# Kernel tuning notes

Measured on AMD Instinct MI355X. Metric: run time of the kernel, lower is better.

## Reference

```python
import jax, jax.numpy as jnp
import numpy as np
import math

H = 128  # hidden_dim
RADIUS = 30.0


def _lin(x, w, b):
    return x @ w + b


def _masked_softmax(logits, mask):
    return jax.nn.softmax(jnp.where(mask, logits, -1e9), axis=-1)


def setup_inputs() -> dict:
    key = jax.random.key(0)
    ks = iter(jax.random.split(key, 64))

    def p(shape, s=0.02):
        return (jax.random.normal(next(ks), shape, jnp.float32) * s)

    B, N, T, M, L = 2, 48, 24, 192, 20
    inp = {
        'agents_state': jax.random.normal(next(ks), (B, N, T, 5), jnp.float32),
        'agents_mask': jnp.ones((B, N, T), jnp.float32),
        'map_polylines': jax.random.normal(next(ks), (B, M, L, 2), jnp.float32),
        'map_poly_mask': jnp.ones((B, M), jnp.float32),
        'map_poly_type': jax.random.randint(next(ks), (B, M), 0, 4),
        'map_tl_status': jax.random.randint(next(ks), (B, M), 0, 8),
        'map_on_route': jax.random.randint(next(ks), (B, M), 0, 2),
        # AgentStateEncoder
        'ae_w0': p((5, H)), 'ae_b0': p((H,)), 'ae_w1': p((H, H)), 'ae_b1': p((H,)),
        'ae_w2': p((H, H)), 'ae_b2': p((H,)),
        # MapPolylineNodeEncoder point_mlp
        'mp_w0': p((2, H)), 'mp_b0': p((H,)), 'mp_w1': p((H, H)), 'mp_b1': p((H,)),
        'type_emb': p((4, H)), 'tl_emb': p((8, H)), 'route_emb': p((2, H)),
        'mo_w0': p((H, H)), 'mo_b0': p((H,)), 'mo_w1': p((H, H)), 'mo_b1': p((H,)),
        # map_rel_mlp (3 -> H -> 1)
        'mr_w0': p((3, H)), 'mr_b0': p((H,)), 'mr_w1': p((H, 1)), 'mr_b1': p((1,)),
        # nbr_rel_mlp (5 -> H -> 1)
        'nr_w0': p((5, H)), 'nr_b0': p((H,)), 'nr_w1': p((H, 1)), 'nr_b1': p((1,)),
        # tau_out (3H -> H -> 64)
        'to_w0': p((3 * H, H)), 'to_b0': p((H,)), 'to_w1': p((H, 64)), 'to_b1': p((64,)),
    }
    return inp


def reference(agents_state, agents_mask, map_polylines, map_poly_mask,
              map_poly_type, map_tl_status, map_on_route,
              ae_w0, ae_b0, ae_w1, ae_b1, ae_w2, ae_b2,
              mp_w0, mp_b0, mp_w1, mp_b1, type_emb, tl_emb, route_emb,
              mo_w0, mo_b0, mo_w1, mo_b1,
              mr_w0, mr_b0, mr_w1, mr_b1,
              nr_w0, nr_b0, nr_w1, nr_b1,
              to_w0, to_b0, to_w1, to_b1):
    B, N, T, _ = agents_state.shape
    a_mask = agents_mask > 0.5
    a_feat = agents_state[..., :5]

    # --- MapPolylineNodeEncoder ---
    m = map_poly_mask > 0.5
    h = jax.nn.relu(_lin(jax.nn.relu(_lin(map_polylines, mp_w0, mp_b0)), mp_w1, mp_b1))  # B,M,L,H
    h = h.max(axis=2)  # B,M,H
    pt = jnp.clip(map_poly_type, 0, type_emb.shape[0] - 1)
    tl = jnp.clip(map_tl_status, 0, tl_emb.shape[0] - 1)
    rt = jnp.clip(map_on_route, 0, route_emb.shape[0] - 1)
    h = h + type_emb[pt] + tl_emb[tl] + route_emb[rt]
    h = _lin(jax.nn.relu(_lin(h, mo_w0, mo_b0)), mo_w1, mo_b1)
    map_node = h * m[..., None].astype(h.dtype)  # B,M,D
    map_center = map_polylines.mean(axis=2)  # B,M,2

    # --- AgentStateEncoder ---
    a = jax.nn.relu(_lin(a_feat, ae_w0, ae_b0))
    a = jax.nn.relu(_lin(a, ae_w1, ae_b1))
    a_emb = _lin(a, ae_w2, ae_b2) * a_mask[..., None].astype(a.dtype)  # B,N,T,D

    # --- map cross-attention with relative-position bias ---
    agent_pos = a_feat[..., 0:2]
    rel = map_center[:, None, None, :, :] - agent_pos[:, :, :, None, :]  # B,N,T,M,2
    dist = jnp.linalg.norm(rel, axis=-1, keepdims=True)
    rel_feat = jnp.concatenate([rel, dist], axis=-1)  # B,N,T,M,3
    rel_score = _lin(jax.nn.relu(_lin(rel_feat, mr_w0, mr_b0)), mr_w1, mr_b1)[..., 0]  # B,N,T,M
    dot = jnp.einsum('bntd,bmd->bntm', a_emb, map_node) / math.sqrt(map_node.shape[-1])
    attn = _masked_softmax(dot + rel_score, m[:, None, None, :])
    map_ctx = jnp.einsum('bntm,bmd->bntd', attn, map_node)

    # --- neighbor graph attention ---
    pos = a_feat[..., 0:2]
    vel = a_feat[..., 3:5]
    rel_pos = jnp.transpose(pos[:, :, None] - pos[:, None, :], (0, 1, 3, 2, 4))  # B,N,T,N,2
    rel_vel = jnp.transpose(vel[:, :, None] - vel[:, None, :], (0, 1, 3, 2, 4))
    dist_ij = jnp.linalg.norm(rel_pos, axis=-1, keepdims=True)  # B,N,T,N,1
    rel_ij = jnp.concatenate([rel_pos, rel_vel, dist_ij], axis=-1)  # B,N,T,N,5
    nbr_score = _lin(jax.nn.relu(_lin(rel_ij, nr_w0, nr_b0)), nr_w1, nr_b1)[..., 0]  # B,N,T,N

    valid_i = a_mask[..., None]  # B,N,T,1
    valid_j = jnp.transpose(a_mask, (0, 2, 1))[:, None, :, :]  # B,1,T,N
    radius_ok = dist_ij[..., 0] <= RADIUS
    not_self = ~jnp.eye(N, dtype=bool)[None, :, None, :]  # 1,N,1,N
    nbr_mask = valid_i & valid_j & radius_ok & not_self

    dot_n = jnp.einsum('bntd,bjtd->bntj', a_emb, a_emb) / math.sqrt(a_emb.shape[-1])
    w_n = _masked_softmax(dot_n + nbr_score, nbr_mask)  # B,N,T,N
    nbr_ctx = jnp.einsum('bntj,bjtd->bntd', w_n, a_emb)

    tau = jnp.concatenate([a_emb, map_ctx, nbr_ctx], axis=-1)
    tau = _lin(jax.nn.relu(_lin(tau, to_w0, to_b0)), to_w1, to_b1)
    tau = tau * a_mask[..., None].astype(tau.dtype)
    return tau, map_ctx, nbr_ctx
```

## Files before the change

### kernel.cpp

```cpp
#include <hip/hip_runtime.h>
#include <math.h>

#define HH 128
#define BB 2
#define NN 48
#define TT 24
#define MM 192
#define LL 20
#define NT (BB*NN*TT)
#define RSQRT_H 0.08838834764831845f
#define RADIUS_C 30.0f

struct P {
    const float *astate, *amask, *polylines, *poly_mask;
    const int *ptype, *tlst, *route;
    const float *ae_w0,*ae_b0,*ae_w1,*ae_b1,*ae_w2,*ae_b2;
    const float *mp_w0,*mp_b0,*mp_w1,*mp_b1;
    const float *type_emb,*tl_emb,*route_emb;
    const float *mo_w0,*mo_b0,*mo_w1,*mo_b1;
    const float *mr_w0,*mr_b0,*mr_w1,*mr_b1;
    const float *nr_w0,*nr_b0,*nr_w1,*nr_b1;
    const float *to_w0,*to_b0,*to_w1,*to_b1;
    float *tau,*map_ctx,*nbr_ctx;
    float *a_emb,*map_node,*map_nodeT,*map_center;
};

struct SME { float pts[LL*2]; float h1[LL][HH]; float mx[2][HH]; float hb[HH]; float pr[2][HH]; float hb2[HH]; };
struct SAG { float xin[4][5]; float h1[4][HH]; float h2[4][HH]; float p1[2][4][HH]; };

struct SF {
    float4 aq4L[HH];
    float  mctx[4][HH];
    float  nctx[4][HH];
    float  pc[2][4][HH];
    union {
        struct {
            float  mnL[16][MM];
            float4 w4L[HH];
            float  w1L[HH];
            float  lg[4][MM];
            float4 p4L[MM];
            float  invL[4];
        } m;
        struct {
            float  pjL[NN][8];
            float4 wAL[HH];
            float4 wBL[HH];
            float  sPL[4][4][NN];
            float  dPL[4][4][NN];
            float  lgN[4][NN];
            float4 pN[NN];
        } n;
        struct {
            float  xinT[3*HH][4];
            float  h1T[HH][4];
        } t;
    } u;
};

__device__ void do_map_enc(const P& p, SME& s, int bm) {
    int tid = threadIdx.x, pp = tid >> 7, c = tid & 127;
    if (tid < LL*2) s.pts[tid] = p.polylines[(size_t)bm*LL*2 + tid];
    __syncthreads();
    {
        float w0x = p.mp_w0[c], w0y = p.mp_w0[HH + c], b0 = p.mp_b0[c];
        #pragma unroll
        for (int i = 0; i < 10; ++i) {
            int pt_ = pp + 2*i;
            s.h1[pt_][c] = fmaxf(fmaf(s.pts[2*pt_], w0x, fmaf(s.pts[2*pt_+1], w0y, b0)), 0.f);
        }
    }
    if (tid < 2) {
        float sum = 0.f;
        for (int q = 0; q < LL; ++q) sum += s.pts[2*q + tid];
        p.map_center[bm*2 + tid] = sum * (1.0f / LL);
    }
    __syncthreads();
    {
        float acc[10];
        float b1 = p.mp_b1[c];
        #pragma unroll
        for (int i = 0; i < 10; ++i) acc[i] = b1;
        for (int k = 0; k < HH; ++k) {
            float wv = p.mp_w1[k*HH + c];
            #pragma unroll
            for (int i = 0; i < 10; ++i) acc[i] = fmaf(s.h1[pp + 2*i][k], wv, acc[i]);
        }
        float m10 = acc[0];
        #pragma unroll
        for (int i = 1; i < 10; ++i) m10 = fmaxf(m10, acc[i]);
        s.mx[pp][c] = m10;
    }
    __syncthreads();
    if (tid < HH) {
        float hm = fmaxf(fmaxf(s.mx[0][c], s.mx[1][c]), 0.f);
        int pt = p.ptype[bm]; pt = pt < 0 ? 0 : (pt > 3 ? 3 : pt);
        int tv = p.tlst[bm];  tv = tv < 0 ? 0 : (tv > 7 ? 7 : tv);
        int rv = p.route[bm]; rv = rv < 0 ? 0 : (rv > 1 ? 1 : rv);
        hm += p.type_emb[pt*HH + c] + p.tl_emb[tv*HH + c] + p.route_emb[rv*HH + c];
        s.hb[c] = hm;
    }
    __syncthreads();
    {
        float sum = 0.f;
        int k0 = pp*64;
        for (int k = k0; k < k0 + 64; ++k) sum = fmaf(s.hb[k], p.mo_w0[k*HH + c], sum);
        s.pr[pp][c] = sum;
    }
    __syncthreads();
    if (tid < HH) s.hb2[c] = fmaxf(s.pr[0][c] + s.pr[1][c] + p.mo_b0[c], 0.f);
    __syncthreads();
    {
        float sum = 0.f;
        int k0 = pp*64;
        for (int k = k0; k < k0 + 64; ++k) sum = fmaf(s.hb2[k], p.mo_w1[k*HH + c], sum);
        s.pr[pp][c] = sum;
    }
    __syncthreads();
    if (tid < HH) {
        float a3 = s.pr[0][c] + s.pr[1][c] + p.mo_b1[c];
        float mk = (p.poly_mask[bm] > 0.5f) ? 1.f : 0.f;
        float v = a3 * mk;
        p.map_node[(size_t)bm*HH + c] = v;
        int b = bm / MM, m = bm % MM;
        p.map_nodeT[((size_t)b*HH + c)*MM + m] = v;
    }
}

__device__ void do_agent_enc(const P& p, SAG& s, int r0) {
    int tid = threadIdx.x, h = tid >> 7, c = tid & 127;
    if (tid < 20) s.xin[tid/5][tid%5] = p.astate[(size_t)r0*5 + tid];
    __syncthreads();
    if (h == 0) {
        float b = p.ae_b0[c];
        float w[5];
        #pragma unroll
        for (int i = 0; i < 5; ++i) w[i] = p.ae_w0[i*HH + c];
        #pragma unroll
        for (int r = 0; r < 4; ++r) {
            float v = b;
            #pragma unroll
            for (int i = 0; i < 5; ++i) v = fmaf(s.xin[r][i], w[i], v);
            s.h1[r][c] = fmaxf(v, 0.f);
        }
    }
    __syncthreads();
    {
        float acc[4] = {0.f,0.f,0.f,0.f};
        int k0 = h*64;
        for (int k = k0; k < k0 + 64; ++k) {
            float wv = p.ae_w1[k*HH + c];
            #pragma unroll
            for (int r = 0; r < 4; ++r) acc[r] = fmaf(s.h1[r][k], wv, acc[r]);
        }
        #pragma unroll
        for (int r = 0; r < 4; ++r) s.p1[h][r][c] = acc[r];
    }
    __syncthreads();
    {
        #pragma unroll
        for (int rr = 0; rr < 2; ++rr) {
            int r = h*2 + rr;
            s.h2[r][c] = fmaxf(s.p1[0][r][c] + s.p1[1][r][c] + p.ae_b1[c], 0.f);
        }
    }
    __syncthreads();
    {
        float acc[4] = {0.f,0.f,0.f,0.f};
        int k0 = h*64;
        for (int k = k0; k < k0 + 64; ++k) {
            float wv = p.ae_w2[k*HH + c];
            #pragma unroll
            for (int r = 0; r < 4; ++r) acc[r] = fmaf(s.h2[r][k], wv, acc[r]);
        }
        #pragma unroll
        for (int r = 0; r < 4; ++r) s.p1[h][r][c] = acc[r];
    }
    __syncthreads();
    {
        #pragma unroll
        for (int rr = 0; rr < 2; ++rr) {
            int r = h*2 + rr;
            int row = r0 + r;
            p.a_emb[(size_t)row*HH + c] = (s.p1[0][r][c] + s.p1[1][r][c] + p.ae_b2[c]) * p.amask[row];
        }
    }
}

__global__ __launch_bounds__(256) void k_enc(P p) {
    __shared__ __align__(16) char smraw[(sizeof(SME) > sizeof(SAG)) ? sizeof(SME) : sizeof(SAG)];
    int task = blockIdx.x;
    if (task < BB*MM) do_map_enc(p, *(SME*)smraw, task);
    else              do_agent_enc(p, *(SAG*)smraw, (task - BB*MM)*4);
}

__global__ __launch_bounds__(256) void k_fat(P p) {
    __shared__ __align__(16) SF s;
    int task = blockIdx.x;
    int b    = task / (TT*12);
    int rem  = task % (TT*12);
    int t    = rem / 12;
    int n0   = (rem % 12) * 4;
    int tid  = threadIdx.x;

    int row0 = (b*NN + n0)*TT + t;

    for (int idx = tid; idx < 4*HH; idx += 256) {
        int r = idx >> 7, k = idx & 127;
        ((float*)&s.aq4L[k])[r] = p.a_emb[(size_t)(row0 + r*TT)*HH + k];
    }
    if (tid < HH) {
        int k = tid;
        s.u.m.w4L[k] = make_float4(p.mr_w0[k], p.mr_w0[HH+k], p.mr_w0[2*HH+k], p.mr_b0[k]);
        s.u.m.w1L[k] = p.mr_w1[k];
    }

    float rx[4], ry[4], rd[4];
    if (tid < MM) {
        float mcx = p.map_center[(b*MM + tid)*2];
        float mcy = p.map_center[(b*MM + tid)*2 + 1];
        #pragma unroll
        for (int r = 0; r < 4; ++r) {
            float px = p.astate[(size_t)(row0 + r*TT)*5];
            float py = p.astate[(size_t)(row0 + r*TT)*5 + 1];
            rx[r] = mcx - px; ry[r] = mcy - py;
            rd[r] = sqrtf(rx[r]*rx[r] + ry[r]*ry[r]);
        }
    }

    const float* mnT = p.map_nodeT + (size_t)b*HH*MM;
    float4 st[3];
    #pragma unroll
    for (int i = 0; i < 3; ++i) {
        int q = tid + 256*i;
        int kk = q / 48, mq = q % 48;
        st[i] = *(const float4*)(mnT + (size_t)kk*MM + mq*4);
    }
    float sacc[4] = {0.f,0.f,0.f,0.f};
    float dt4[4]  = {0.f,0.f,0.f,0.f};
    for (int ch = 0; ch < 8; ++ch) {
        __syncthreads();
        #pragma unroll
        for (int i = 0; i < 3; ++i) {
            int q = tid + 256*i;
            int kk = q / 48, mq = q % 48;
            *(float4*)&s.u.m.mnL[kk][mq*4] = st[i];
        }
        __syncthreads();
        if (ch < 7) {
            #pragma unroll
            for (int i = 0; i < 3; ++i) {
                int q = tid + 256*i;
                int kk = q / 48, mq = q % 48;
                st[i] = *(const float4*)(mnT + (size_t)(ch+1)*16*MM + (size_t)kk*MM + mq*4);
            }
        }
        if (tid < MM) {
            int k0 = ch*16;
            #pragma unroll
            for (int kk = 0; kk < 16; ++kk) {
                int k = k0 + kk;
                float4 w  = s.u.m.w4L[k];
                float  w1 = s.u.m.w1L[k];
                float4 aq = s.aq4L[k];
                float  mn = s.u.m.mnL[kk][tid];
                #pragma unroll
                for (int r = 0; r < 4; ++r) {
                    float hv = fmaf(rx[r], w.x, fmaf(ry[r], w.y, fmaf(rd[r], w.z, w.w)));
                    sacc[r] = fmaf(fmaxf(hv, 0.f), w1, sacc[r]);
                }
                dt4[0] = fmaf(aq.x, mn, dt4[0]);
                dt4[1] = fmaf(aq.y, mn, dt4[1]);
                dt4[2] = fmaf(aq.z, mn, dt4[2]);
                dt4[3] = fmaf(aq.w, mn, dt4[3]);
            }
        }
    }
    if (tid < MM) {
        float pm = p.poly_mask[b*MM + tid];
        float b1 = p.mr_b1[0];
        #pragma unroll
        for (int r = 0; r < 4; ++r) {
            float lgt = fmaf(dt4[r], RSQRT_H, sacc[r] + b1);
            s.u.m.lg[r][tid] = (pm > 0.5f) ? lgt : -1e9f;
        }
    }
    __syncthreads();

    {
        int r = tid >> 6, l = tid & 63;
        float v = fmaxf(fmaxf(s.u.m.lg[r][l], s.u.m.lg[r][l+64]), s.u.m.lg[r][l+128]);
        #pragma unroll
        for (int o = 32; o > 0; o >>= 1) v = fmaxf(v, __shfl_xor(v, o));
        float e0 = expf(s.u.m.lg[r][l] - v);
        float e1 = expf(s.u.m.lg[r][l+64] - v);
        float e2 = expf(s.u.m.lg[r][l+128] - v);
        s.u.m.lg[r][l] = e0; s.u.m.lg[r][l+64] = e1; s.u.m.lg[r][l+128] = e2;
        float sm = e0 + e1 + e2;
        #pragma unroll
        for (int o = 32; o > 0; o >>= 1) sm += __shfl_xor(sm, o);
        if (l == 0) s.u.m.invL[r] = 1.0f / sm;
    }
    __syncthreads();
    if (tid < MM) {
        s.u.m.p4L[tid] = make_float4(s.u.m.lg[0][tid]*s.u.m.invL[0], s.u.m.lg[1][tid]*s.u.m.invL[1],
                                     s.u.m.lg[2][tid]*s.u.m.invL[2], s.u.m.lg[3][tid]*s.u.m.invL[3]);
    }
    __syncthreads();

    {
        int half = tid >> 7, c = tid & 127;
        float a0=0.f, a1=0.f, a2=0.f, a3=0.f;
        const float* mnb = p.map_node + ((size_t)b*MM + half*96)*HH + c;
        for (int m = 0; m < 96; ++m) {
            float mv = mnb[(size_t)m*HH];
            float4 pp4 = s.u.m.p4L[half*96 + m];
            a0 = fmaf(pp4.x, mv, a0); a1 = fmaf(pp4.y, mv, a1);
            a2 = fmaf(pp4.z, mv, a2); a3 = fmaf(pp4.w, mv, a3);
        }
        s.pc[half][0][c]=a0; s.pc[half][1][c]=a1; s.pc[half][2][c]=a2; s.pc[half][3][c]=a3;
    }
    __syncthreads();
    for (int idx = tid; idx < 4*HH; idx += 256) {
        int r = idx >> 7, c = idx & 127;
        float v = s.pc[0][r][c] + s.pc[1][r][c];
        s.mctx[r][c] = v;
        p.map_ctx[(size_t)(row0 + r*TT)*HH + c] = v;
    }
    __syncthreads();

    if (tid < NN) {
        int rj = (b*NN + tid)*TT + t;
        s.u.n.pjL[tid][0] = p.astate[(size_t)rj*5];
        s.u.n.pjL[tid][1] = p.astate[(size_t)rj*5 + 1];
        s.u.n.pjL[tid][2] = p.astate[(size_t)rj*5 + 3];
        s.u.n.pjL[tid][3] = p.astate[(size_t)rj*5 + 4];
        s.u.n.pjL[tid][4] = p.amask[rj];
    }
    if (tid < HH) {
        int k = tid;
        s.u.n.wAL[k] = make_float4(p.nr_w0[k], p.nr_w0[HH+k], p.nr_w0[2*HH+k], p.nr_w0[3*HH+k]);
        s.u.n.wBL[k] = make_float4(p.nr_w0[4*HH+k], p.nr_b0[k], p.nr_w1[k], 0.f);
    }
    __syncthreads();

    {
        int j  = tid % 48;
        int kg = tid / 48;
        if (kg < 4) {
            float jx = s.u.n.pjL[j][0], jy = s.u.n.pjL[j][1];
            float jvx = s.u.n.pjL[j][2], jvy = s.u.n.pjL[j][3];
            float dx[4], dy[4], dvx[4], dvy[4], dd[4];
            #pragma unroll
            for (int r = 0; r < 4; ++r) {
                int ni = n0 + r;
                dx[r]  = s.u.n.pjL[ni][0] - jx;  dy[r]  = s.u.n.pjL[ni][1] - jy;
                dvx[r] = s.u.n.pjL[ni][2] - jvx; dvy[r] = s.u.n.pjL[ni][3] - jvy;
                dd[r]  = sqrtf(dx[r]*dx[r] + dy[r]*dy[r]);
            }
            const float* aj = p.a_emb + ((size_t)(b*NN + j)*TT + t)*HH;
            float sr[4]  = {0,0,0,0};
            float dtn[4] = {0,0,0,0};
            int k0 = kg*32;
            for (int kk = 0; kk < 32; ++kk) {
                int k = k0 + kk;
                float4 wa = s.u.n.wAL[k], wb = s.u.n.wBL[k];
                float4 aq = s.aq4L[k];
                float  av = aj[k];
                #pragma unroll
                for (int r = 0; r < 4; ++r) {
                    float hv = fmaf(dx[r], wa.x, fmaf(dy[r], wa.y,
                               fmaf(dvx[r], wa.z, fmaf(dvy[r], wa.w,
                               fmaf(dd[r], wb.x, wb.y)))));
                    sr[r] = fmaf(fmaxf(hv, 0.f), wb.z, sr[r]);
                }
                dtn[0] = fmaf(aq.x, av, dtn[0]); dtn[1] = fmaf(aq.y, av, dtn[1]);
                dtn[2] = fmaf(aq.z, av, dtn[2]); dtn[3] = fmaf(aq.w, av, dtn[3]);
            }
            #pragma unroll
            for (int r = 0; r < 4; ++r) { s.u.n.sPL[kg][r][j] = sr[r]; s.u.n.dPL[kg][r][j] = dtn[r]; }
        }
    }
    __syncthreads();

    {
        float b1 = p.nr_b1[0];
        for (int idx = tid; idx < 4*NN; idx += 256) {
            int r = idx / NN, jj = idx % NN;
            int ni = n0 + r;
            float ss  = s.u.n.sPL[0][r][jj] + s.u.n.sPL[1][r][jj] + s.u.n.sPL[2][r][jj] + s.u.n.sPL[3][r][jj] + b1;
            float do2 = s.u.n.dPL[0][r][jj] + s.u.n.dPL[1][r][jj] + s.u.n.dPL[2][r][jj] + s.u.n.dPL[3][r][jj];
            float ddx = s.u.n.pjL[ni][0] - s.u.n.pjL[jj][0];
            float ddy = s.u.n.pjL[ni][1] - s.u.n.pjL[jj][1];
            float dist = sqrtf(ddx*ddx + ddy*ddy);
            bool ok = (s.u.n.pjL[ni][4] > 0.5f) && (s.u.n.pjL[jj][4] > 0.5f) &&
                      (dist <= RADIUS_C) && (jj != ni);
            s.u.n.lgN[r][jj] = ok ? fmaf(do2, RSQRT_H, ss) : -1e9f;
        }
    }
    __syncthreads();

    {
        int r = tid >> 6, l = tid & 63;
        float v = (l < NN) ? s.u.n.lgN[r][l] : -3.4e38f;
        #pragma unroll
        for (int o = 32; o > 0; o >>= 1) v = fmaxf(v, __shfl_xor(v, o));
        float e = (l < NN) ? expf(s.u.n.lgN[r][l] - v) : 0.f;
        float sm = e;
        #pragma unroll
        for (int o = 32; o > 0; o >>= 1) sm += __shfl_xor(sm, o);
        if (l < NN) s.u.n.lgN[r][l] = e / sm;
    }
    __syncthreads();
    if (tid < NN) {
        s.u.n.pN[tid] = make_float4(s.u.n.lgN[0][tid], s.u.n.lgN[1][tid],
                                    s.u.n.lgN[2][tid], s.u.n.lgN[3][tid]);
    }
    __syncthreads();

    {
        int half = tid >> 7, c = tid & 127;
        float a0=0.f, a1=0.f, a2=0.f, a3=0.f;
        for (int jj = half*24; jj < half*24 + 24; ++jj) {
            float av = p.a_emb[((size_t)(b*NN + jj)*TT + t)*HH + c];
            float4 pp4 = s.u.n.pN[jj];
            a0 = fmaf(pp4.x, av, a0); a1 = fmaf(pp4.y, av, a1);
            a2 = fmaf(pp4.z, av, a2); a3 = fmaf(pp4.w, av, a3);
        }
        s.pc[half][0][c]=a0; s.pc[half][1][c]=a1; s.pc[half][2][c]=a2; s.pc[half][3][c]=a3;
    }
    __syncthreads();
    for (int idx = tid; idx < 4*HH; idx += 256) {
        int r = idx >> 7, c = idx & 127;
        float v = s.pc[0][r][c] + s.pc[1][r][c];
        s.nctx[r][c] = v;
        p.nbr_ctx[(size_t)(row0 + r*TT)*HH + c] = v;
    }
    __syncthreads();

    for (int idx = tid; idx < 4*HH; idx += 256) {
        int r = idx >> 7, k = idx & 127;
        s.u.t.xinT[k][r]        = ((float*)&s.aq4L[k])[r];
        s.u.t.xinT[HH + k][r]   = s.mctx[r][k];
        s.u.t.xinT[2*HH + k][r] = s.nctx[r][k];
    }
    __syncthreads();
    {
        int c = tid & 127, h = tid >> 7;
        float acc[4] = {0,0,0,0};
        for (int k = h*192; k < h*192 + 192; ++k) {
            float wv = p.to_w0[k*HH + c];
            float4 xa = *(const float4*)&s.u.t.xinT[k][0];
            acc[0]=fmaf(xa.x,wv,acc[0]); acc[1]=fmaf(xa.y,wv,acc[1]);
            acc[2]=fmaf(xa.z,wv,acc[2]); acc[3]=fmaf(xa.w,wv,acc[3]);
        }
        #pragma unroll
        for (int r = 0; r < 4; ++r) s.pc[h][r][c] = acc[r];
    }
    __syncthreads();
    for (int idx = tid; idx < 4*HH; idx += 256) {
        int r = idx >> 7, k = idx & 127;
        s.u.t.h1T[k][r] = fmaxf(s.pc[0][r][k] + s.pc[1][r][k] + p.to_b0[k], 0.f);
    }
    __syncthreads();
    {
        int r = tid >> 6, c2 = tid & 63;
        float acc = p.to_b1[c2];
        for (int k = 0; k < HH; ++k)
            acc = fmaf(s.u.t.h1T[k][r], p.to_w1[k*64 + c2], acc);
        p.tau[(size_t)(row0 + r*TT)*64 + c2] = acc * p.amask[row0 + r*TT];
    }
}

extern "C" void kernel_launch(void* const* d_in, const int* in_sizes, int n_in,
                              void* d_out, int out_size, void* d_ws, size_t ws_size,
                              hipStream_t stream)
{
    P p;
    p.astate    = (const float*)d_in[0];
    p.amask     = (const float*)d_in[1];
    p.polylines = (const float*)d_in[2];
    p.poly_mask = (const float*)d_in[3];
    p.ptype     = (const int*)d_in[4];
    p.tlst      = (const int*)d_in[5];
    p.route     = (const int*)d_in[6];
    p.ae_w0 = (const float*)d_in[7];  p.ae_b0 = (const float*)d_in[8];
    p.ae_w1 = (const float*)d_in[9];  p.ae_b1 = (const float*)d_in[10];
    p.ae_w2 = (const float*)d_in[11]; p.ae_b2 = (const float*)d_in[12];
    p.mp_w0 = (const float*)d_in[13]; p.mp_b0 = (const float*)d_in[14];
    p.mp_w1 = (const float*)d_in[15]; p.mp_b1 = (const float*)d_in[16];
    p.type_emb  = (const float*)d_in[17];
    p.tl_emb    = (const float*)d_in[18];
    p.route_emb = (const float*)d_in[19];
    p.mo_w0 = (const float*)d_in[20]; p.mo_b0 = (const float*)d_in[21];
    p.mo_w1 = (const float*)d_in[22]; p.mo_b1 = (const float*)d_in[23];
    p.mr_w0 = (const float*)d_in[24]; p.mr_b0 = (const float*)d_in[25];
    p.mr_w1 = (const float*)d_in[26]; p.mr_b1 = (const float*)d_in[27];
    p.nr_w0 = (const float*)d_in[28]; p.nr_b0 = (const float*)d_in[29];
    p.nr_w1 = (const float*)d_in[30]; p.nr_b1 = (const float*)d_in[31];
    p.to_w0 = (const float*)d_in[32]; p.to_b0 = (const float*)d_in[33];
    p.to_w1 = (const float*)d_in[34]; p.to_b1 = (const float*)d_in[35];

    p.tau     = (float*)d_out;
    p.map_ctx = (float*)d_out + (size_t)NT*64;
    p.nbr_ctx = p.map_ctx + (size_t)NT*HH;

    float* ws    = (float*)d_ws;
    p.a_emb      = ws;
    p.map_node   = p.a_emb + (size_t)NT*HH;
    p.map_nodeT  = p.map_node + (size_t)BB*MM*HH;
    p.map_center = p.map_nodeT + (size_t)BB*MM*HH;

    k_enc<<<BB*MM + NT/4, 256, 0, stream>>>(p);
    k_fat<<<BB*TT*12,     256, 0, stream>>>(p);
}
```

Baseline: 187.9 us.

## Halve rows per block to double grid size and drop shared map tiling

Each block in both kernels now handles 2 agent rows instead of 4, doubling the number of blocks (576 to 1152 for the fat kernel and more agent-encoder blocks) to fill more compute units. The map logit loop drops the staged shared-memory tiles of map_nodeT and reads it directly from global memory with coalesced per-thread loads. The final tau projection is split across both thread halves over k. This gives more parallelism and less shared memory per block, but weight loads are reused across fewer rows, so global and L2 traffic per output grows.

```diff
diff --git a/kernel.cpp b/kernel.cpp
--- a/kernel.cpp
+++ b/kernel.cpp
@@ -26,34 +26,33 @@
 };
 
 struct SME { float pts[LL*2]; float h1[LL][HH]; float mx[2][HH]; float hb[HH]; float pr[2][HH]; float hb2[HH]; };
-struct SAG { float xin[4][5]; float h1[4][HH]; float h2[4][HH]; float p1[2][4][HH]; };
+struct SAG { float xin[2][5]; float h1[2][HH]; float h2[2][HH]; float p1[2][2][HH]; };
 
 struct SF {
-    float4 aq4L[HH];
-    float  mctx[4][HH];
-    float  nctx[4][HH];
-    float  pc[2][4][HH];
+    float aqL[HH][2];
+    float mctx[2][HH];
+    float nctx[2][HH];
+    float pc[2][2][HH];
     union {
         struct {
-            float  mnL[16][MM];
             float4 w4L[HH];
             float  w1L[HH];
-            float  lg[4][MM];
-            float4 p4L[MM];
-            float  invL[4];
+            float  lg[2][MM];
+            float  p2[MM][2];
+            float  invL[2];
         } m;
         struct {
             float  pjL[NN][8];
             float4 wAL[HH];
             float4 wBL[HH];
-            float  sPL[4][4][NN];
-            float  dPL[4][4][NN];
-            float  lgN[4][NN];
-            float4 pN[NN];
+            float  sPL[4][2][NN];
+            float  dPL[4][2][NN];
+            float  lgN[2][NN];
+            float  pN[NN][2];
         } n;
         struct {
-            float  xinT[3*HH][4];
-            float  h1T[HH][4];
+            float  xinT[3*HH][2];
+            float  h1T[HH][2];
         } t;
     } u;
 };
@@ -129,7 +128,7 @@
 
 __device__ void do_agent_enc(const P& p, SAG& s, int r0) {
     int tid = threadIdx.x, h = tid >> 7, c = tid & 127;
-    if (tid < 20) s.xin[tid/5][tid%5] = p.astate[(size_t)r0*5 + tid];
+    if (tid < 10) s.xin[tid/5][tid%5] = p.astate[(size_t)r0*5 + tid];
     __syncthreads();
     if (h == 0) {
         float b = p.ae_b0[c];
@@ -137,7 +136,7 @@
         #pragma unroll
         for (int i = 0; i < 5; ++i) w[i] = p.ae_w0[i*HH + c];
         #pragma unroll
-        for (int r = 0; r < 4; ++r) {
+        for (int r = 0; r < 2; ++r) {
             float v = b;
             #pragma unroll
             for (int i = 0; i < 5; ++i) v = fmaf(s.xin[r][i], w[i], v);
@@ -146,44 +145,36 @@
     }
     __syncthreads();
     {
-        float acc[4] = {0.f,0.f,0.f,0.f};
+        float a0 = 0.f, a1 = 0.f;
         int k0 = h*64;
         for (int k = k0; k < k0 + 64; ++k) {
             float wv = p.ae_w1[k*HH + c];
-            #pragma unroll
-            for (int r = 0; r < 4; ++r) acc[r] = fmaf(s.h1[r][k], wv, acc[r]);
-        }
-        #pragma unroll
-        for (int r = 0; r < 4; ++r) s.p1[h][r][c] = acc[r];
-    }
-    __syncthreads();
-    {
-        #pragma unroll
-        for (int rr = 0; rr < 2; ++rr) {
-            int r = h*2 + rr;
-            s.h2[r][c] = fmaxf(s.p1[0][r][c] + s.p1[1][r][c] + p.ae_b1[c], 0.f);
-        }
-    }
-    __syncthreads();
-    {
-        float acc[4] = {0.f,0.f,0.f,0.f};
+            a0 = fmaf(s.h1[0][k], wv, a0);
+            a1 = fmaf(s.h1[1][k], wv, a1);
+        }
+        s.p1[h][0][c] = a0; s.p1[h][1][c] = a1;
+    }
+    __syncthreads();
+    {
+        int r = h;
+        s.h2[r][c] = fmaxf(s.p1[0][r][c] + s.p1[1][r][c] + p.ae_b1[c], 0.f);
+    }
+    __syncthreads();
+    {
+        float a0 = 0.f, a1 = 0.f;
         int k0 = h*64;
         for (int k = k0; k < k0 + 64; ++k) {
             float wv = p.ae_w2[k*HH + c];
-            #pragma unroll
-            for (int r = 0; r < 4; ++r) acc[r] = fmaf(s.h2[r][k], wv, acc[r]);
-        }
-        #pragma unroll
-        for (int r = 0; r < 4; ++r) s.p1[h][r][c] = acc[r];
-    }
-    __syncthreads();
-    {
-        #pragma unroll
-        for (int rr = 0; rr < 2; ++rr) {
-            int r = h*2 + rr;
-            int row = r0 + r;
-            p.a_emb[(size_t)row*HH + c] = (s.p1[0][r][c] + s.p1[1][r][c] + p.ae_b2[c]) * p.amask[row];
-        }
+            a0 = fmaf(s.h2[0][k], wv, a0);
+            a1 = fmaf(s.h2[1][k], wv, a1);
+        }
+        s.p1[h][0][c] = a0; s.p1[h][1][c] = a1;
+    }
+    __syncthreads();
+    {
+        int r = h;
+        int row = r0 + r;
+        p.a_emb[(size_t)row*HH + c] = (s.p1[0][r][c] + s.p1[1][r][c] + p.ae_b2[c]) * p.amask[row];
     }
 }
 
@@ -191,23 +182,23 @@
     __shared__ __align__(16) char smraw[(sizeof(SME) > sizeof(SAG)) ? sizeof(SME) : sizeof(SAG)];
     int task = blockIdx.x;
     if (task < BB*MM) do_map_enc(p, *(SME*)smraw, task);
-    else              do_agent_enc(p, *(SAG*)smraw, (task - BB*MM)*4);
+    else              do_agent_enc(p, *(SAG*)smraw, (task - BB*MM)*2);
 }
 
 __global__ __launch_bounds__(256) void k_fat(P p) {
     __shared__ __align__(16) SF s;
     int task = blockIdx.x;
-    int b    = task / (TT*12);
-    int rem  = task % (TT*12);
-    int t    = rem / 12;
-    int n0   = (rem % 12) * 4;
+    int b    = task / (TT*24);
+    int rem  = task % (TT*24);
+    int t    = rem / 24;
+    int n0   = (rem % 24) * 2;
     int tid  = threadIdx.x;
 
     int row0 = (b*NN + n0)*TT + t;
 
-    for (int idx = tid; idx < 4*HH; idx += 256) {
-        int r = idx >> 7, k = idx & 127;
-        ((float*)&s.aq4L[k])[r] = p.a_emb[(size_t)(row0 + r*TT)*HH + k];
+    for (int idx = tid; idx < 2*HH; idx += 256) {
+        int r = idx & 1, k = idx >> 1;
+        s.aqL[k][r] = p.a_emb[(size_t)(row0 + r*TT)*HH + k];
     }
     if (tid < HH) {
         int k = tid;
@@ -215,113 +206,86 @@
         s.u.m.w1L[k] = p.mr_w1[k];
     }
 
-    float rx[4], ry[4], rd[4];
+    float rx[2], ry[2], rd[2];
     if (tid < MM) {
         float mcx = p.map_center[(b*MM + tid)*2];
         float mcy = p.map_center[(b*MM + tid)*2 + 1];
         #pragma unroll
-        for (int r = 0; r < 4; ++r) {
+        for (int r = 0; r < 2; ++r) {
             float px = p.astate[(size_t)(row0 + r*TT)*5];
             float py = p.astate[(size_t)(row0 + r*TT)*5 + 1];
             rx[r] = mcx - px; ry[r] = mcy - py;
             rd[r] = sqrtf(rx[r]*rx[r] + ry[r]*ry[r]);
         }
     }
-
-    const float* mnT = p.map_nodeT + (size_t)b*HH*MM;
-    float4 st[3];
-    #pragma unroll
-    for (int i = 0; i < 3; ++i) {
-        int q = tid + 256*i;
-        int kk = q / 48, mq = q % 48;
-        st[i] = *(const float4*)(mnT + (size_t)kk*MM + mq*4);
-    }
-    float sacc[4] = {0.f,0.f,0.f,0.f};
-    float dt4[4]  = {0.f,0.f,0.f,0.f};
-    for (int ch = 0; ch < 8; ++ch) {
-        __syncthreads();
-        #pragma unroll
-        for (int i = 0; i < 3; ++i) {
-            int q = tid + 256*i;
-            int kk = q / 48, mq = q % 48;
-            *(float4*)&s.u.m.mnL[kk][mq*4] = st[i];
-        }
-        __syncthreads();
-        if (ch < 7) {
-            #pragma unroll
-            for (int i = 0; i < 3; ++i) {
-                int q = tid + 256*i;
-                int kk = q / 48, mq = q % 48;
-                st[i] = *(const float4*)(mnT + (size_t)(ch+1)*16*MM + (size_t)kk*MM + mq*4);
+    __syncthreads();
+
+    if (tid < MM) {
+        const float* mnc = p.map_nodeT + (size_t)b*HH*MM + tid;
+        float sacc[2] = {0.f, 0.f};
+        float dt2[2]  = {0.f, 0.f};
+        #pragma unroll 8
+        for (int k = 0; k < HH; ++k) {
+            float4 w  = s.u.m.w4L[k];
+            float  w1 = s.u.m.w1L[k];
+            float  mn = mnc[(size_t)k*MM];
+            float  aq0 = s.aqL[k][0], aq1 = s.aqL[k][1];
+            #pragma unroll
+            for (int r = 0; r < 2; ++r) {
+                float hv = fmaf(rx[r], w.x, fmaf(ry[r], w.y, fmaf(rd[r], w.z, w.w)));
+                sacc[r] = fmaf(fmaxf(hv, 0.f), w1, sacc[r]);
             }
-        }
-        if (tid < MM) {
-            int k0 = ch*16;
-            #pragma unroll
-            for (int kk = 0; kk < 16; ++kk) {
-                int k = k0 + kk;
-                float4 w  = s.u.m.w4L[k];
-                float  w1 = s.u.m.w1L[k];
-                float4 aq = s.aq4L[k];
-                float  mn = s.u.m.mnL[kk][tid];
-                #pragma unroll
-                for (int r = 0; r < 4; ++r) {
-                    float hv = fmaf(rx[r], w.x, fmaf(ry[r], w.y, fmaf(rd[r], w.z, w.w)));
-                    sacc[r] = fmaf(fmaxf(hv, 0.f), w1, sacc[r]);
-                }
-                dt4[0] = fmaf(aq.x, mn, dt4[0]);
-                dt4[1] = fmaf(aq.y, mn, dt4[1]);
-                dt4[2] = fmaf(aq.z, mn, dt4[2]);
-                dt4[3] = fmaf(aq.w, mn, dt4[3]);
-            }
-        }
-    }
-    if (tid < MM) {
+            dt2[0] = fmaf(aq0, mn, dt2[0]);
+            dt2[1] = fmaf(aq1, mn, dt2[1]);
+        }
         float pm = p.poly_mask[b*MM + tid];
         float b1 = p.mr_b1[0];
         #pragma unroll
-        for (int r = 0; r < 4; ++r) {
-            float lgt = fmaf(dt4[r], RSQRT_H, sacc[r] + b1);
+        for (int r = 0; r < 2; ++r) {
+            float lgt = fmaf(dt2[r], RSQRT_H, sacc[r] + b1);
             s.u.m.lg[r][tid] = (pm > 0.5f) ? lgt : -1e9f;
         }
     }
     __syncthreads();
 
     {
-        int r = tid >> 6, l = tid & 63;
-        float v = fmaxf(fmaxf(s.u.m.lg[r][l], s.u.m.lg[r][l+64]), s.u.m.lg[r][l+128]);
-        #pragma unroll
-        for (int o = 32; o > 0; o >>= 1) v = fmaxf(v, __shfl_xor(v, o));
-        float e0 = expf(s.u.m.lg[r][l] - v);
-        float e1 = expf(s.u.m.lg[r][l+64] - v);
-        float e2 = expf(s.u.m.lg[r][l+128] - v);
-        s.u.m.lg[r][l] = e0; s.u.m.lg[r][l+64] = e1; s.u.m.lg[r][l+128] = e2;
-        float sm = e0 + e1 + e2;
-        #pragma unroll
-        for (int o = 32; o > 0; o >>= 1) sm += __shfl_xor(sm, o);
-        if (l == 0) s.u.m.invL[r] = 1.0f / sm;
+        int w = tid >> 6, l = tid & 63;
+        if (w < 2) {
+            int r = w;
+            float v = fmaxf(fmaxf(s.u.m.lg[r][l], s.u.m.lg[r][l+64]), s.u.m.lg[r][l+128]);
+            #pragma unroll
+            for (int o = 32; o > 0; o >>= 1) v = fmaxf(v, __shfl_xor(v, o));
+            float e0 = expf(s.u.m.lg[r][l] - v);
+            float e1 = expf(s.u.m.lg[r][l+64] - v);
+            float e2 = expf(s.u.m.lg[r][l+128] - v);
+            s.u.m.lg[r][l] = e0; s.u.m.lg[r][l+64] = e1; s.u.m.lg[r][l+128] = e2;
+            float sm = e0 + e1 + e2;
+            #pragma unroll
+            for (int o = 32; o > 0; o >>= 1) sm += __shfl_xor(sm, o);
+            if (l == 0) s.u.m.invL[r] = 1.0f / sm;
+        }
     }
     __syncthreads();
     if (tid < MM) {
-        s.u.m.p4L[tid] = make_float4(s.u.m.lg[0][tid]*s.u.m.invL[0], s.u.m.lg[1][tid]*s.u.m.invL[1],
-                                     s.u.m.lg[2][tid]*s.u.m.invL[2], s.u.m.lg[3][tid]*s.u.m.invL[3]);
+        s.u.m.p2[tid][0] = s.u.m.lg[0][tid] * s.u.m.invL[0];
+        s.u.m.p2[tid][1] = s.u.m.lg[1][tid] * s.u.m.invL[1];
     }
     __syncthreads();
 
     {
         int half = tid >> 7, c = tid & 127;
-        float a0=0.f, a1=0.f, a2=0.f, a3=0.f;
+        float a0 = 0.f, a1 = 0.f;
         const float* mnb = p.map_node + ((size_t)b*MM + half*96)*HH + c;
         for (int m = 0; m < 96; ++m) {
             float mv = mnb[(size_t)m*HH];
-            float4 pp4 = s.u.m.p4L[half*96 + m];
-            a0 = fmaf(pp4.x, mv, a0); a1 = fmaf(pp4.y, mv, a1);
-            a2 = fmaf(pp4.z, mv, a2); a3 = fmaf(pp4.w, mv, a3);
-        }
-        s.pc[half][0][c]=a0; s.pc[half][1][c]=a1; s.pc[half][2][c]=a2; s.pc[half][3][c]=a3;
-    }
-    __syncthreads();
-    for (int idx = tid; idx < 4*HH; idx += 256) {
+            float p0 = s.u.m.p2[half*96 + m][0];
+            float p1v = s.u.m.p2[half*96 + m][1];
+            a0 = fmaf(p0, mv, a0); a1 = fmaf(p1v, mv, a1);
+        }
+        s.pc[half][0][c] = a0; s.pc[half][1][c] = a1;
+    }
+    __syncthreads();
+    for (int idx = tid; idx < 2*HH; idx += 256) {
         int r = idx >> 7, c = idx & 127;
         float v = s.pc[0][r][c] + s.pc[1][r][c];
         s.mctx[r][c] = v;
@@ -350,42 +314,43 @@
         if (kg < 4) {
             float jx = s.u.n.pjL[j][0], jy = s.u.n.pjL[j][1];
             float jvx = s.u.n.pjL[j][2], jvy = s.u.n.pjL[j][3];
-            float dx[4], dy[4], dvx[4], dvy[4], dd[4];
-            #pragma unroll
-            for (int r = 0; r < 4; ++r) {
+            float dx[2], dy[2], dvx[2], dvy[2], dd[2];
+            #pragma unroll
+            for (int r = 0; r < 2; ++r) {
                 int ni = n0 + r;
                 dx[r]  = s.u.n.pjL[ni][0] - jx;  dy[r]  = s.u.n.pjL[ni][1] - jy;
                 dvx[r] = s.u.n.pjL[ni][2] - jvx; dvy[r] = s.u.n.pjL[ni][3] - jvy;
                 dd[r]  = sqrtf(dx[r]*dx[r] + dy[r]*dy[r]);
             }
             const float* aj = p.a_emb + ((size_t)(b*NN + j)*TT + t)*HH;
-            float sr[4]  = {0,0,0,0};
-            float dtn[4] = {0,0,0,0};
+            float sr[2]  = {0.f, 0.f};
+            float dtn[2] = {0.f, 0.f};
             int k0 = kg*32;
+            #pragma unroll 8
             for (int kk = 0; kk < 32; ++kk) {
                 int k = k0 + kk;
                 float4 wa = s.u.n.wAL[k], wb = s.u.n.wBL[k];
-                float4 aq = s.aq4L[k];
                 float  av = aj[k];
+                float  aq0 = s.aqL[k][0], aq1 = s.aqL[k][1];
                 #pragma unroll
-                for (int r = 0; r < 4; ++r) {
+                for (int r = 0; r < 2; ++r) {
                     float hv = fmaf(dx[r], wa.x, fmaf(dy[r], wa.y,
                                fmaf(dvx[r], wa.z, fmaf(dvy[r], wa.w,
                                fmaf(dd[r], wb.x, wb.y)))));
                     sr[r] = fmaf(fmaxf(hv, 0.f), wb.z, sr[r]);
                 }
-                dtn[0] = fmaf(aq.x, av, dtn[0]); dtn[1] = fmaf(aq.y, av, dtn[1]);
-                dtn[2] = fmaf(aq.z, av, dtn[2]); dtn[3] = fmaf(aq.w, av, dtn[3]);
+                dtn[0] = fmaf(aq0, av, dtn[0]);
+                dtn[1] = fmaf(aq1, av, dtn[1]);
             }
             #pragma unroll
-            for (int r = 0; r < 4; ++r) { s.u.n.sPL[kg][r][j] = sr[r]; s.u.n.dPL[kg][r][j] = dtn[r]; }
+            for (int r = 0; r < 2; ++r) { s.u.n.sPL[kg][r][j] = sr[r]; s.u.n.dPL[kg][r][j] = dtn[r]; }
         }
     }
     __syncthreads();
 
     {
         float b1 = p.nr_b1[0];
-        for (int idx = tid; idx < 4*NN; idx += 256) {
+        for (int idx = tid; idx < 2*NN; idx += 256) {
             int r = idx / NN, jj = idx % NN;
             int ni = n0 + r;
             float ss  = s.u.n.sPL[0][r][jj] + s.u.n.sPL[1][r][jj] + s.u.n.sPL[2][r][jj] + s.u.n.sPL[3][r][jj] + b1;
@@ -401,36 +366,38 @@
     __syncthreads();
 
     {
-        int r = tid >> 6, l = tid & 63;
-        float v = (l < NN) ? s.u.n.lgN[r][l] : -3.4e38f;
-        #pragma unroll
-        for (int o = 32; o > 0; o >>= 1) v = fmaxf(v, __shfl_xor(v, o));
-        float e = (l < NN) ? expf(s.u.n.lgN[r][l] - v) : 0.f;
-        float sm = e;
-        #pragma unroll
-        for (int o = 32; o > 0; o >>= 1) sm += __shfl_xor(sm, o);
-        if (l < NN) s.u.n.lgN[r][l] = e / sm;
+        int w = tid >> 6, l = tid & 63;
+        if (w < 2) {
+            int r = w;
+            float v = (l < NN) ? s.u.n.lgN[r][l] : -3.4e38f;
+            #pragma unroll
+            for (int o = 32; o > 0; o >>= 1) v = fmaxf(v, __shfl_xor(v, o));
+            float e = (l < NN) ? expf(s.u.n.lgN[r][l] - v) : 0.f;
+            float sm = e;
+            #pragma unroll
+            for (int o = 32; o > 0; o >>= 1) sm += __shfl_xor(sm, o);
+            if (l < NN) s.u.n.lgN[r][l] = e / sm;
+        }
     }
     __syncthreads();
     if (tid < NN) {
-        s.u.n.pN[tid] = make_float4(s.u.n.lgN[0][tid], s.u.n.lgN[1][tid],
-                                    s.u.n.lgN[2][tid], s.u.n.lgN[3][tid]);
+        s.u.n.pN[tid][0] = s.u.n.lgN[0][tid];
+        s.u.n.pN[tid][1] = s.u.n.lgN[1][tid];
     }
     __syncthreads();
 
     {
         int half = tid >> 7, c = tid & 127;
-        float a0=0.f, a1=0.f, a2=0.f, a3=0.f;
+        float a0 = 0.f, a1 = 0.f;
         for (int jj = half*24; jj < half*24 + 24; ++jj) {
             float av = p.a_emb[((size_t)(b*NN + jj)*TT + t)*HH + c];
-            float4 pp4 = s.u.n.pN[jj];
-            a0 = fmaf(pp4.x, av, a0); a1 = fmaf(pp4.y, av, a1);
-            a2 = fmaf(pp4.z, av, a2); a3 = fmaf(pp4.w, av, a3);
-        }
-        s.pc[half][0][c]=a0; s.pc[half][1][c]=a1; s.pc[half][2][c]=a2; s.pc[half][3][c]=a3;
-    }
-    __syncthreads();
-    for (int idx = tid; idx < 4*HH; idx += 256) {
+            a0 = fmaf(s.u.n.pN[jj][0], av, a0);
+            a1 = fmaf(s.u.n.pN[jj][1], av, a1);
+        }
+        s.pc[half][0][c] = a0; s.pc[half][1][c] = a1;
+    }
+    __syncthreads();
+    for (int idx = tid; idx < 2*HH; idx += 256) {
         int r = idx >> 7, c = idx & 127;
         float v = s.pc[0][r][c] + s.pc[1][r][c];
         s.nctx[r][c] = v;
@@ -438,37 +405,45 @@
     }
     __syncthreads();
 
-    for (int idx = tid; idx < 4*HH; idx += 256) {
-        int r = idx >> 7, k = idx & 127;
-        s.u.t.xinT[k][r]        = ((float*)&s.aq4L[k])[r];
+    for (int idx = tid; idx < 2*HH; idx += 256) {
+        int r = idx & 1, k = idx >> 1;
+        s.u.t.xinT[k][r]        = s.aqL[k][r];
         s.u.t.xinT[HH + k][r]   = s.mctx[r][k];
         s.u.t.xinT[2*HH + k][r] = s.nctx[r][k];
     }
     __syncthreads();
     {
         int c = tid & 127, h = tid >> 7;
-        float acc[4] = {0,0,0,0};
+        float a0 = 0.f, a1 = 0.f;
+        #pragma unroll 8
         for (int k = h*192; k < h*192 + 192; ++k) {
             float wv = p.to_w0[k*HH + c];
-            float4 xa = *(const float4*)&s.u.t.xinT[k][0];
-            acc[0]=fmaf(xa.x,wv,acc[0]); acc[1]=fmaf(xa.y,wv,acc[1]);
-            acc[2]=fmaf(xa.z,wv,acc[2]); acc[3]=fmaf(xa.w,wv,acc[3]);
-        }
-        #pragma unroll
-        for (int r = 0; r < 4; ++r) s.pc[h][r][c] = acc[r];
-    }
-    __syncthreads();
-    for (int idx = tid; idx < 4*HH; idx += 256) {
-        int r = idx >> 7, k = idx & 127;
+            float x0 = s.u.t.xinT[k][0], x1 = s.u.t.xinT[k][1];
+            a0 = fmaf(x0, wv, a0);
+            a1 = fmaf(x1, wv, a1);
+        }
+        s.pc[h][0][c] = a0; s.pc[h][1][c] = a1;
+    }
+    __syncthreads();
+    for (int idx = tid; idx < 2*HH; idx += 256) {
+        int r = idx & 1, k = idx >> 1;
         s.u.t.h1T[k][r] = fmaxf(s.pc[0][r][k] + s.pc[1][r][k] + p.to_b0[k], 0.f);
     }
     __syncthreads();
     {
+        int kh = tid >> 7, rc = tid & 127;
+        int r = rc >> 6, c2 = rc & 63;
+        float acc = 0.f;
+        for (int k = kh*64; k < kh*64 + 64; ++k)
+            acc = fmaf(s.u.t.h1T[k][r], p.to_w1[k*64 + c2], acc);
+        s.pc[kh][r][c2] = acc;
+    }
+    __syncthreads();
+    if (tid < 128) {
         int r = tid >> 6, c2 = tid & 63;
-        float acc = p.to_b1[c2];
-        for (int k = 0; k < HH; ++k)
-            acc = fmaf(s.u.t.h1T[k][r], p.to_w1[k*64 + c2], acc);
-        p.tau[(size_t)(row0 + r*TT)*64 + c2] = acc * p.amask[row0 + r*TT];
+        int row = row0 + r*TT;
+        float v = (s.pc[0][r][c2] + s.pc[1][r][c2] + p.to_b1[c2]) * p.amask[row];
+        p.tau[(size_t)row*64 + c2] = v;
     }
 }
 
@@ -511,6 +486,6 @@
     p.map_nodeT  = p.map_node + (size_t)BB*MM*HH;
     p.map_center = p.map_nodeT + (size_t)BB*MM*HH;
 
-    k_enc<<<BB*MM + NT/4, 256, 0, stream>>>(p);
-    k_fat<<<BB*TT*12,     256, 0, stream>>>(p);
+    k_enc<<<BB*MM + NT/2, 256, 0, stream>>>(p);
+    k_fat<<<BB*TT*24,     256, 0, stream>>>(p);
 }
```

After: 184.5 us. No clear change (-1.8%).
